# Kernel tuning notes

Hardware: AMD Instinct MI355X
Metric: run time of the kernel (lower is better)

## Reference

```python
import jax, jax.numpy as jnp
import numpy as np

H = 16  # num_heads (matches init_kwargs)


def setup_inputs() -> dict:
    key = jax.random.key(0)
    ks = jax.random.split(key, 5)
    B, T, C = 4, 2048, 2048
    S = C // H
    g = 0.5 * (6.0 / (C + C)) ** 0.5 * (3.0 ** 0.5)  # ~xavier_uniform scale, gain 0.5
    x = jax.random.normal(ks[0], (B, T, C), dtype=jnp.float32)
    Wk = jax.random.uniform(ks[1], (C, C), jnp.float32, -g, g)
    Wv = jax.random.uniform(ks[2], (C, C), jnp.float32, -g, g)
    Wr = jax.random.uniform(ks[3], (C, C), jnp.float32, -g, g)
    Wo = jax.random.uniform(ks[4], (C, C), jnp.float32, -g, g)
    time_decay = jnp.full((H, S), -5.0, dtype=jnp.float32)
    time_first = jnp.zeros((H, S), dtype=jnp.float32)
    return {"x": x, "Wk": Wk, "Wv": Wv, "Wr": Wr, "Wo": Wo,
            "time_decay": time_decay, "time_first": time_first}


def _wkv(k, v, time_decay, time_first):
    # k, v: [B, T, H, S] float32
    decay = jnp.exp(-jnp.exp(time_decay.astype(jnp.float32)))  # [H, S]
    first = jnp.exp(time_first.astype(jnp.float32))            # [H, S]
    w = jnp.exp(jnp.clip(k.astype(jnp.float32), -10.0, 10.0))  # [B, T, H, S]
    # t==0 branch (state = first*w0*v0) == uniform recurrence with w0 scaled by first
    w = w.at[:, 0].multiply(first)
    wt = jnp.swapaxes(w, 0, 1)                    # [T, B, H, S]
    vt = jnp.swapaxes(v.astype(jnp.float32), 0, 1)

    def step(carry, inp):
        num, den = carry
        w_t, v_t = inp
        num = decay * num + w_t * v_t
        den = decay * den + w_t
        return (num, den), num / (den + 1e-6)

    B, _, _, S = k.shape
    init = (jnp.zeros((B, H, S), jnp.float32), jnp.zeros((B, H, S), jnp.float32))
    _, wkv = jax.lax.scan(step, init, (wt, vt))   # [T, B, H, S]
    return jnp.swapaxes(wkv, 0, 1).astype(k.dtype)  # [B, T, H, S]


def reference(x, Wk, Wv, Wr, Wo, time_decay, time_first):
    B, T, C = x.shape
    S = C // H
    k = (x @ Wk.T).reshape(B, T, H, S)
    v = (x @ Wv.T).reshape(B, T, H, S)
    r = (x @ Wr.T).reshape(B, T, H, S)
    wkv = _wkv(k, v, time_decay, time_first)
    rwkv = (jax.nn.sigmoid(r) * wkv).reshape(B, T, C)
    return rwkv @ Wo.T
```

## Files before the change

### kernel.cpp

```cpp
#include <hip/hip_runtime.h>
#include <hip/hip_bf16.h>

using bf16 = __hip_bfloat16;
using floatx4 = __attribute__((ext_vector_type(4))) float;
using bf16x8  = __attribute__((ext_vector_type(8))) __bf16;
using bf16x2  = __attribute__((ext_vector_type(2))) __bf16;

#define MDIM 8192
#define NDIM 2048
#define KDIM 2048
#define TSEQ 2048
#define BB   4
#define CDIM 2048
#define NCHUNK 64
#define TCHUNK 32

typedef __attribute__((address_space(1))) void gvoid_t;
typedef __attribute__((address_space(3))) void lvoid_t;

__device__ __forceinline__ void load_lds16(const void* g, void* l) {
  __builtin_amdgcn_global_load_lds((gvoid_t*)(void*)g, (lvoid_t*)l, 16, 0, 0);
}

__global__ __launch_bounds__(256) void cvt_all(
    const float* __restrict__ x,
    const float* __restrict__ Wk, const float* __restrict__ Wv,
    const float* __restrict__ Wr, const float* __restrict__ Wo,
    __bf16* __restrict__ xb,
    __bf16* __restrict__ wkb, __bf16* __restrict__ wvb,
    __bf16* __restrict__ wrb, __bf16* __restrict__ wob) {
  const size_t WN = (size_t)NDIM * KDIM;
  const int slice = blockIdx.y;
  const float* s;
  __bf16* d;
  if (slice < 4) { s = x + (size_t)slice * WN; d = xb + (size_t)slice * WN; }
  else {
    s = (slice == 4) ? Wk : (slice == 5) ? Wv : (slice == 6) ? Wr : Wo;
    d = (slice == 4) ? wkb : (slice == 5) ? wvb : (slice == 6) ? wrb : wob;
  }
  const int i = (blockIdx.x * 256 + threadIdx.x) * 8;
  float4 a = *(const float4*)(s + i);
  float4 b = *(const float4*)(s + i + 4);
  bf16x8 o;
  o[0] = (__bf16)a.x; o[1] = (__bf16)a.y; o[2] = (__bf16)a.z; o[3] = (__bf16)a.w;
  o[4] = (__bf16)b.x; o[5] = (__bf16)b.y; o[6] = (__bf16)b.z; o[7] = (__bf16)b.w;
  *(bf16x8*)(d + i) = o;
}


#define GBARRIER() asm volatile("s_barrier" ::: "memory")
#define VMW8()     asm volatile("s_waitcnt vmcnt(8)" ::: "memory")
#define VMW4()     asm volatile("s_waitcnt vmcnt(4)" ::: "memory")
#define VMW0()     asm volatile("s_waitcnt vmcnt(0)" ::: "memory")

template <typename CT>
__device__ __forceinline__ void gemm256_body(const __bf16* __restrict__ A,
                                             const __bf16* __restrict__ B,
                                             CT* __restrict__ C,
                                             const int bm, const int bn) {
  __shared__ __attribute__((aligned(128))) unsigned char lds[131072];
  const int tid  = threadIdx.x;
  const int lane = tid & 63;
  const int wave = tid >> 6;
  const int wm = wave >> 2;
  const int wn = wave & 3;

  floatx4 acc[8][4] = {};
  bf16x8 af[8], bfr[2];

  const int srow = tid >> 2;
  const int scol = ((tid & 3) ^ ((tid >> 3) & 3)) * 8;
  const __bf16* Ag = A + (size_t)(bm * 256 + srow) * KDIM + scol;
  const __bf16* Bg = B + (size_t)(bn * 256 + srow) * KDIM + scol;
  const uint32_t sdst = (uint32_t)tid * 16u;

  const uint32_t laneoff =
      (uint32_t)((lane & 15) * 64 + (((lane >> 4) ^ ((lane >> 1) & 3)) * 16));
  const uint32_t aoff = (uint32_t)(wm * 8192) + laneoff;
  const uint32_t boff = 16384u + (uint32_t)(wn * 4096) + laneoff;

#define BUF(t_) ((uint32_t)((t_) & 3) * 32768u)
#define STG_A(t_) {                                                           \
  load_lds16(Ag + (size_t)(t_) * 32,                                          \
             (void*)(lds + BUF(t_) + sdst));                                  \
  load_lds16(Ag + (size_t)128 * KDIM + (size_t)(t_) * 32,                     \
             (void*)(lds + BUF(t_) + 8192u + sdst)); }
#define STG_B(t_) {                                                           \
  load_lds16(Bg + (size_t)(t_) * 32,                                          \
             (void*)(lds + BUF(t_) + 16384u + sdst));                         \
  load_lds16(Bg + (size_t)128 * KDIM + (size_t)(t_) * 32,                     \
             (void*)(lds + BUF(t_) + 24576u + sdst)); }
#define RD_AF(bo_) {                                                          \
  const uint32_t ab = (bo_) + aoff;                                           \
  af[0] = *(const bf16x8*)(lds + ab);        af[1] = *(const bf16x8*)(lds + ab + 1024); \
  af[2] = *(const bf16x8*)(lds + ab + 2048); af[3] = *(const bf16x8*)(lds + ab + 3072); \
  af[4] = *(const bf16x8*)(lds + ab + 4096); af[5] = *(const bf16x8*)(lds + ab + 5120); \
  af[6] = *(const bf16x8*)(lds + ab + 6144); af[7] = *(const bf16x8*)(lds + ab + 7168); }
#define RD_BF(bo_, nh_) {                                                     \
  const uint32_t bb = (bo_) + boff + (nh_) * 2048u;                           \
  bfr[0] = *(const bf16x8*)(lds + bb);                                        \
  bfr[1] = *(const bf16x8*)(lds + bb + 1024); }
#define MFMA16(j0_) {                                                         \
  __builtin_amdgcn_s_setprio(1);                                              \
  _Pragma("unroll")                                                           \
  for (int m_ = 0; m_ < 8; ++m_) {                                            \
    acc[m_][(j0_)]     = __builtin_amdgcn_mfma_f32_16x16x32_bf16(af[m_], bfr[0], acc[m_][(j0_)], 0, 0, 0);     \
    acc[m_][(j0_) + 1] = __builtin_amdgcn_mfma_f32_16x16x32_bf16(af[m_], bfr[1], acc[m_][(j0_) + 1], 0, 0, 0); \
  }                                                                           \
  __builtin_amdgcn_s_setprio(0); }

  STG_A(0); STG_B(0);
  STG_A(1); STG_B(1);
  STG_A(2); STG_B(2);
  VMW8();
  GBARRIER();

  constexpr int NT = KDIM / 32;
  for (int t = 0; t < NT - 3; ++t) {
    const uint32_t bo = BUF(t);
    RD_AF(bo); RD_BF(bo, 0);
    STG_A(t + 3);
    MFMA16(0);
    RD_BF(bo, 1);
    STG_B(t + 3);
    MFMA16(2);
    VMW8();
    GBARRIER();
  }
  {
    const uint32_t bo = BUF(NT - 3);
    RD_AF(bo); RD_BF(bo, 0);
    MFMA16(0);
    RD_BF(bo, 1);
    MFMA16(2);
    VMW4();
    GBARRIER();
  }
  {
    const uint32_t bo = BUF(NT - 2);
    RD_AF(bo); RD_BF(bo, 0);
    MFMA16(0);
    RD_BF(bo, 1);
    MFMA16(2);
    VMW0();
    GBARRIER();
  }
  {
    const uint32_t bo = BUF(NT - 1);
    RD_AF(bo); RD_BF(bo, 0);
    MFMA16(0);
    RD_BF(bo, 1);
    MFMA16(2);
  }

  const int crow = (lane >> 4) * 4;
  const int ccol = lane & 15;
#pragma unroll
  for (int i = 0; i < 8; ++i)
#pragma unroll
    for (int j = 0; j < 4; ++j) {
      const size_t r0 = (size_t)(bm * 256 + wm * 128 + i * 16 + crow);
      const int    c0 = bn * 256 + wn * 64 + j * 16 + ccol;
#pragma unroll
      for (int rg = 0; rg < 4; ++rg)
        C[(r0 + rg) * NDIM + c0] = (CT)(acc[i][j][rg]);
    }
#undef BUF
#undef STG_A
#undef STG_B
#undef RD_AF
#undef RD_BF
#undef MFMA16
}

__device__ __forceinline__ void xcd_swz(int& bm, int& bn) {
  const int f = (int)(blockIdx.y * 32 + blockIdx.x);
  const int s = (f & 7) * 32 + (f >> 3);
  bm = s & 31;
  bn = s >> 5;
}

__global__ __launch_bounds__(512, 2) void gemm_qkv(const __bf16* __restrict__ x,
                                                   const __bf16* __restrict__ Wk,
                                                   const __bf16* __restrict__ Wv,
                                                   const __bf16* __restrict__ Wr,
                                                   __bf16* __restrict__ kb,
                                                   __bf16* __restrict__ vb,
                                                   __bf16* __restrict__ rb) {
  const __bf16* Bsel = (blockIdx.z == 0) ? Wk : (blockIdx.z == 1) ? Wv : Wr;
  __bf16*       Csel = (blockIdx.z == 0) ? kb : (blockIdx.z == 1) ? vb : rb;
  int bm, bn; xcd_swz(bm, bn);
  gemm256_body<__bf16>(x, Bsel, Csel, bm, bn);
}

__global__ __launch_bounds__(512, 2) void gemm_o(const __bf16* __restrict__ A,
                                                 const __bf16* __restrict__ B,
                                                 float* __restrict__ C) {
  int bm, bn; xcd_swz(bm, bn);
  gemm256_body<float>(A, B, C, bm, bn);
}

__global__ __launch_bounds__(256) void wkv_summary(
    const __bf16* __restrict__ kb, const __bf16* __restrict__ vb,
    const float* __restrict__ td, const float* __restrict__ tf,
    float* __restrict__ nsum, float* __restrict__ dsum) {
  const int c0 = (blockIdx.x * 256 + threadIdx.x) * 2;
  const int chunk = blockIdx.y;
  const int b = blockIdx.z;
  const float dc0 = __expf(-__expf(td[c0]));
  const float dc1 = __expf(-__expf(td[c0 + 1]));
  const float fi0 = __expf(tf[c0]);
  const float fi1 = __expf(tf[c0 + 1]);
  size_t base = ((size_t)b * TSEQ + (size_t)chunk * TCHUNK) * CDIM + c0;
  float n0 = 0.f, d0 = 0.f, n1 = 0.f, d1 = 0.f;
#pragma unroll 4
  for (int t = 0; t < TCHUNK; ++t) {
    bf16x2 k2 = *(const bf16x2*)(kb + base + (size_t)t * CDIM);
    bf16x2 v2 = *(const bf16x2*)(vb + base + (size_t)t * CDIM);
    float k0f = fminf(fmaxf((float)k2[0], -10.f), 10.f);
    float k1f = fminf(fmaxf((float)k2[1], -10.f), 10.f);
    float w0 = __expf(k0f), w1 = __expf(k1f);
    if (chunk == 0 && t == 0) { w0 *= fi0; w1 *= fi1; }
    n0 = dc0 * n0 + w0 * (float)v2[0];
    d0 = dc0 * d0 + w0;
    n1 = dc1 * n1 + w1 * (float)v2[1];
    d1 = dc1 * d1 + w1;
  }
  const size_t si = (size_t)(chunk * BB + b) * CDIM + c0;
  *(float2*)(nsum + si) = make_float2(n0, n1);
  *(float2*)(dsum + si) = make_float2(d0, d1);
}

__global__ __launch_bounds__(256) void wkv_scan(
    const float* __restrict__ td,
    float* __restrict__ nsum, float* __restrict__ dsum) {
  const int c0 = (blockIdx.x * 256 + threadIdx.x) * 2;
  const int b = blockIdx.y;
  const float dT0 = __expf(-__expf(td[c0]) * (float)TCHUNK);
  const float dT1 = __expf(-__expf(td[c0 + 1]) * (float)TCHUNK);
  float pn0 = 0.f, pd0 = 0.f, pn1 = 0.f, pd1 = 0.f;
  for (int j = 0; j < NCHUNK; ++j) {
    const size_t si = (size_t)(j * BB + b) * CDIM + c0;
    float2 Sn = *(const float2*)(nsum + si);
    float2 Sd = *(const float2*)(dsum + si);
    *(float2*)(nsum + si) = make_float2(pn0, pn1);
    *(float2*)(dsum + si) = make_float2(pd0, pd1);
    pn0 = dT0 * pn0 + Sn.x;  pn1 = dT1 * pn1 + Sn.y;
    pd0 = dT0 * pd0 + Sd.x;  pd1 = dT1 * pd1 + Sd.y;
  }
}

__global__ __launch_bounds__(256) void wkv_apply(
    const __bf16* __restrict__ kb, const __bf16* __restrict__ vb,
    __bf16* __restrict__ rb,
    const float* __restrict__ td, const float* __restrict__ tf,
    const float* __restrict__ nsum, const float* __restrict__ dsum) {
  const int c0 = (blockIdx.x * 256 + threadIdx.x) * 2;
  const int chunk = blockIdx.y;
  const int b = blockIdx.z;
  const float dc0 = __expf(-__expf(td[c0]));
  const float dc1 = __expf(-__expf(td[c0 + 1]));
  const float fi0 = __expf(tf[c0]);
  const float fi1 = __expf(tf[c0 + 1]);

  const size_t si = (size_t)(chunk * BB + b) * CDIM + c0;
  float2 pn = *(const float2*)(nsum + si);
  float2 pd = *(const float2*)(dsum + si);
  float n0 = pn.x, n1 = pn.y, d0 = pd.x, d1 = pd.y;

  size_t base = ((size_t)b * TSEQ + (size_t)chunk * TCHUNK) * CDIM + c0;
#pragma unroll 2
  for (int t = 0; t < TCHUNK; ++t) {
    const size_t idx = base + (size_t)t * CDIM;
    bf16x2 k2 = *(const bf16x2*)(kb + idx);
    bf16x2 v2 = *(const bf16x2*)(vb + idx);
    bf16x2 r2 = *(const bf16x2*)(rb + idx);
    float k0f = fminf(fmaxf((float)k2[0], -10.f), 10.f);
    float k1f = fminf(fmaxf((float)k2[1], -10.f), 10.f);
    float w0 = __expf(k0f), w1 = __expf(k1f);
    if (chunk == 0 && t == 0) { w0 *= fi0; w1 *= fi1; }
    n0 = dc0 * n0 + w0 * (float)v2[0];
    d0 = dc0 * d0 + w0;
    n1 = dc1 * n1 + w1 * (float)v2[1];
    d1 = dc1 * d1 + w1;
    const float wkv0 = n0 * __builtin_amdgcn_rcpf(d0 + 1e-6f);
    const float wkv1 = n1 * __builtin_amdgcn_rcpf(d1 + 1e-6f);
    const float sr0 = __builtin_amdgcn_rcpf(1.f + __expf(-(float)r2[0]));
    const float sr1 = __builtin_amdgcn_rcpf(1.f + __expf(-(float)r2[1]));
    bf16x2 o;
    o[0] = (__bf16)(sr0 * wkv0);
    o[1] = (__bf16)(sr1 * wkv1);
    *(bf16x2*)(rb + idx) = o;
  }
}

extern "C" void kernel_launch(void* const* d_in, const int* in_sizes, int n_in,
                              void* d_out, int out_size, void* d_ws, size_t ws_size,
                              hipStream_t stream) {
  const float* x  = (const float*)d_in[0];
  const float* Wk = (const float*)d_in[1];
  const float* Wv = (const float*)d_in[2];
  const float* Wr = (const float*)d_in[3];
  const float* Wo = (const float*)d_in[4];
  const float* td = (const float*)d_in[5];
  const float* tf = (const float*)d_in[6];
  float* out = (float*)d_out;

  char* ws = (char*)d_ws;
  const size_t matX = (size_t)MDIM * KDIM * sizeof(__bf16);
  const size_t matW = (size_t)NDIM * KDIM * sizeof(__bf16);
  __bf16* xb  = (__bf16*)(ws);
  __bf16* wkb = (__bf16*)(ws + matX);
  __bf16* wvb = (__bf16*)(ws + matX + matW);
  __bf16* wrb = (__bf16*)(ws + matX + 2 * matW);
  __bf16* wob = (__bf16*)(ws + matX + 3 * matW);
  __bf16* kb  = (__bf16*)(ws + matX + 4 * matW);
  __bf16* vb  = (__bf16*)(ws + 2 * matX + 4 * matW);
  __bf16* rb  = (__bf16*)(ws + 3 * matX + 4 * matW);
  float* nsum = (float*)(ws + 4 * matX + 4 * matW);
  float* dsum = nsum + (size_t)NCHUNK * BB * CDIM;

  dim3 blk(256);
  dim3 blk5(512);
  cvt_all<<<dim3(NDIM * KDIM / (8 * 256), 8), blk, 0, stream>>>(
      x, Wk, Wv, Wr, Wo, xb, wkb, wvb, wrb, wob);

  dim3 gq(MDIM / 256, NDIM / 256, 3);
  gemm_qkv<<<gq, blk5, 0, stream>>>(xb, wkb, wvb, wrb, kb, vb, rb);
  dim3 gw(CDIM / 512, NCHUNK, BB);
  wkv_summary<<<gw, blk, 0, stream>>>(kb, vb, td, tf, nsum, dsum);
  wkv_scan<<<dim3(CDIM / 512, BB), blk, 0, stream>>>(td, nsum, dsum);
  wkv_apply<<<gw, blk, 0, stream>>>(kb, vb, rb, td, tf, nsum, dsum);
  dim3 go(MDIM / 256, NDIM / 256, 1);
  gemm_o<<<go, blk5, 0, stream>>>(rb, wob, out);
}
```

Measured before the change: 465.8 us.

## Use 4-wave 256x256 GEMM tiles with 128x128 per-wave output

Rebuilds the shared 256x256 bf16 GEMM body so that 4 waves (256 threads) cover the tile instead of 8. Each wave now computes a 128x128 sub-tile with 8x8 MFMA accumulators and reads 8 B fragments per k-step, which raises MFMA work per LDS read. Each thread issues 4 global-to-LDS loads per operand, and the vmcnt waits are adjusted to match. The cost is twice the accumulator registers (256 VGPRs of accumulators) and one block per CU, which risks register spilling and leaves less latency hiding.

```diff
diff --git a/kernel.cpp b/kernel.cpp
--- a/kernel.cpp
+++ b/kernel.cpp
@@ -49,8 +49,8 @@
 
 
 #define GBARRIER() asm volatile("s_barrier" ::: "memory")
+#define VMW16()    asm volatile("s_waitcnt vmcnt(16)" ::: "memory")
 #define VMW8()     asm volatile("s_waitcnt vmcnt(8)" ::: "memory")
-#define VMW4()     asm volatile("s_waitcnt vmcnt(4)" ::: "memory")
 #define VMW0()     asm volatile("s_waitcnt vmcnt(0)" ::: "memory")
 
 template <typename CT>
@@ -62,11 +62,11 @@
   const int tid  = threadIdx.x;
   const int lane = tid & 63;
   const int wave = tid >> 6;
-  const int wm = wave >> 2;
-  const int wn = wave & 3;
-
-  floatx4 acc[8][4] = {};
-  bf16x8 af[8], bfr[2];
+  const int wm = wave >> 1;
+  const int wn = wave & 1;
+
+  floatx4 acc[8][8] = {};
+  bf16x8 af[8], bfr[8];
 
   const int srow = tid >> 2;
   const int scol = ((tid & 3) ^ ((tid >> 3) & 3)) * 8;
@@ -77,80 +77,78 @@
   const uint32_t laneoff =
       (uint32_t)((lane & 15) * 64 + (((lane >> 4) ^ ((lane >> 1) & 3)) * 16));
   const uint32_t aoff = (uint32_t)(wm * 8192) + laneoff;
-  const uint32_t boff = 16384u + (uint32_t)(wn * 4096) + laneoff;
+  const uint32_t boff = 16384u + (uint32_t)(wn * 8192) + laneoff;
 
 #define BUF(t_) ((uint32_t)((t_) & 3) * 32768u)
 #define STG_A(t_) {                                                           \
-  load_lds16(Ag + (size_t)(t_) * 32,                                          \
-             (void*)(lds + BUF(t_) + sdst));                                  \
-  load_lds16(Ag + (size_t)128 * KDIM + (size_t)(t_) * 32,                     \
-             (void*)(lds + BUF(t_) + 8192u + sdst)); }
+  _Pragma("unroll")                                                           \
+  for (int q_ = 0; q_ < 4; ++q_)                                              \
+    load_lds16(Ag + (size_t)(q_ * 64) * KDIM + (size_t)(t_) * 32,             \
+               (void*)(lds + BUF(t_) + (uint32_t)q_ * 4096u + sdst)); }
 #define STG_B(t_) {                                                           \
-  load_lds16(Bg + (size_t)(t_) * 32,                                          \
-             (void*)(lds + BUF(t_) + 16384u + sdst));                         \
-  load_lds16(Bg + (size_t)128 * KDIM + (size_t)(t_) * 32,                     \
-             (void*)(lds + BUF(t_) + 24576u + sdst)); }
+  _Pragma("unroll")                                                           \
+  for (int q_ = 0; q_ < 4; ++q_)                                              \
+    load_lds16(Bg + (size_t)(q_ * 64) * KDIM + (size_t)(t_) * 32,             \
+               (void*)(lds + BUF(t_) + 16384u + (uint32_t)q_ * 4096u + sdst)); }
 #define RD_AF(bo_) {                                                          \
   const uint32_t ab = (bo_) + aoff;                                           \
-  af[0] = *(const bf16x8*)(lds + ab);        af[1] = *(const bf16x8*)(lds + ab + 1024); \
-  af[2] = *(const bf16x8*)(lds + ab + 2048); af[3] = *(const bf16x8*)(lds + ab + 3072); \
-  af[4] = *(const bf16x8*)(lds + ab + 4096); af[5] = *(const bf16x8*)(lds + ab + 5120); \
-  af[6] = *(const bf16x8*)(lds + ab + 6144); af[7] = *(const bf16x8*)(lds + ab + 7168); }
-#define RD_BF(bo_, nh_) {                                                     \
-  const uint32_t bb = (bo_) + boff + (nh_) * 2048u;                           \
-  bfr[0] = *(const bf16x8*)(lds + bb);                                        \
-  bfr[1] = *(const bf16x8*)(lds + bb + 1024); }
-#define MFMA16(j0_) {                                                         \
+  _Pragma("unroll")                                                           \
+  for (int i_ = 0; i_ < 8; ++i_)                                              \
+    af[i_] = *(const bf16x8*)(lds + ab + (uint32_t)i_ * 1024u); }
+#define RD_BF(bo_) {                                                          \
+  const uint32_t bb = (bo_) + boff;                                           \
+  _Pragma("unroll")                                                           \
+  for (int j_ = 0; j_ < 8; ++j_)                                              \
+    bfr[j_] = *(const bf16x8*)(lds + bb + (uint32_t)j_ * 1024u); }
+#define MFMA32(J0_) {                                                         \
   __builtin_amdgcn_s_setprio(1);                                              \
   _Pragma("unroll")                                                           \
-  for (int m_ = 0; m_ < 8; ++m_) {                                            \
-    acc[m_][(j0_)]     = __builtin_amdgcn_mfma_f32_16x16x32_bf16(af[m_], bfr[0], acc[m_][(j0_)], 0, 0, 0);     \
-    acc[m_][(j0_) + 1] = __builtin_amdgcn_mfma_f32_16x16x32_bf16(af[m_], bfr[1], acc[m_][(j0_) + 1], 0, 0, 0); \
+  for (int j_ = (J0_); j_ < (J0_) + 4; ++j_) {                                \
+    _Pragma("unroll")                                                         \
+    for (int m_ = 0; m_ < 8; ++m_)                                            \
+      acc[m_][j_] = __builtin_amdgcn_mfma_f32_16x16x32_bf16(                  \
+          af[m_], bfr[j_], acc[m_][j_], 0, 0, 0);                             \
   }                                                                           \
   __builtin_amdgcn_s_setprio(0); }
 
   STG_A(0); STG_B(0);
   STG_A(1); STG_B(1);
   STG_A(2); STG_B(2);
-  VMW8();
+  VMW16();
   GBARRIER();
 
   constexpr int NT = KDIM / 32;
   for (int t = 0; t < NT - 3; ++t) {
     const uint32_t bo = BUF(t);
-    RD_AF(bo); RD_BF(bo, 0);
+    RD_AF(bo); RD_BF(bo);
     STG_A(t + 3);
-    MFMA16(0);
-    RD_BF(bo, 1);
+    MFMA32(0);
     STG_B(t + 3);
-    MFMA16(2);
+    MFMA32(4);
+    VMW16();
+    GBARRIER();
+  }
+  {
+    const uint32_t bo = BUF(NT - 3);
+    RD_AF(bo); RD_BF(bo);
+    MFMA32(0);
+    MFMA32(4);
     VMW8();
     GBARRIER();
   }
   {
-    const uint32_t bo = BUF(NT - 3);
-    RD_AF(bo); RD_BF(bo, 0);
-    MFMA16(0);
-    RD_BF(bo, 1);
-    MFMA16(2);
-    VMW4();
-    GBARRIER();
-  }
-  {
     const uint32_t bo = BUF(NT - 2);
-    RD_AF(bo); RD_BF(bo, 0);
-    MFMA16(0);
-    RD_BF(bo, 1);
-    MFMA16(2);
+    RD_AF(bo); RD_BF(bo);
+    MFMA32(0);
+    MFMA32(4);
     VMW0();
     GBARRIER();
   }
   {
     const uint32_t bo = BUF(NT - 1);
-    RD_AF(bo); RD_BF(bo, 0);
-    MFMA16(0);
-    RD_BF(bo, 1);
-    MFMA16(2);
+    RD_AF(bo); RD_BF(bo);
+    MFMA32(0);
+    MFMA32(4);
   }
 
   const int crow = (lane >> 4) * 4;
@@ -158,9 +156,9 @@
 #pragma unroll
   for (int i = 0; i < 8; ++i)
 #pragma unroll
-    for (int j = 0; j < 4; ++j) {
+    for (int j = 0; j < 8; ++j) {
       const size_t r0 = (size_t)(bm * 256 + wm * 128 + i * 16 + crow);
-      const int    c0 = bn * 256 + wn * 64 + j * 16 + ccol;
+      const int    c0 = bn * 256 + wn * 128 + j * 16 + ccol;
 #pragma unroll
       for (int rg = 0; rg < 4; ++rg)
         C[(r0 + rg) * NDIM + c0] = (CT)(acc[i][j][rg]);
@@ -170,7 +168,7 @@
 #undef STG_B
 #undef RD_AF
 #undef RD_BF
-#undef MFMA16
+#undef MFMA32
 }
 
 __device__ __forceinline__ void xcd_swz(int& bm, int& bn) {
@@ -180,7 +178,7 @@
   bn = s >> 5;
 }
 
-__global__ __launch_bounds__(512, 2) void gemm_qkv(const __bf16* __restrict__ x,
+__global__ __launch_bounds__(256, 1) void gemm_qkv(const __bf16* __restrict__ x,
                                                    const __bf16* __restrict__ Wk,
                                                    const __bf16* __restrict__ Wv,
                                                    const __bf16* __restrict__ Wr,
@@ -193,7 +191,7 @@
   gemm256_body<__bf16>(x, Bsel, Csel, bm, bn);
 }
 
-__global__ __launch_bounds__(512, 2) void gemm_o(const __bf16* __restrict__ A,
+__global__ __launch_bounds__(256, 1) void gemm_o(const __bf16* __restrict__ A,
                                                  const __bf16* __restrict__ B,
                                                  float* __restrict__ C) {
   int bm, bn; xcd_swz(bm, bn);
@@ -321,16 +319,15 @@
   float* dsum = nsum + (size_t)NCHUNK * BB * CDIM;
 
   dim3 blk(256);
-  dim3 blk5(512);
   cvt_all<<<dim3(NDIM * KDIM / (8 * 256), 8), blk, 0, stream>>>(
       x, Wk, Wv, Wr, Wo, xb, wkb, wvb, wrb, wob);
 
   dim3 gq(MDIM / 256, NDIM / 256, 3);
-  gemm_qkv<<<gq, blk5, 0, stream>>>(xb, wkb, wvb, wrb, kb, vb, rb);
+  gemm_qkv<<<gq, blk, 0, stream>>>(xb, wkb, wvb, wrb, kb, vb, rb);
   dim3 gw(CDIM / 512, NCHUNK, BB);
   wkv_summary<<<gw, blk, 0, stream>>>(kb, vb, td, tf, nsum, dsum);
   wkv_scan<<<dim3(CDIM / 512, BB), blk, 0, stream>>>(td, nsum, dsum);
   wkv_apply<<<gw, blk, 0, stream>>>(kb, vb, rb, td, tf, nsum, dsum);
   dim3 go(MDIM / 256, NDIM / 256, 1);
-  gemm_o<<<go, blk5, 0, stream>>>(rb, wob, out);
-}
+  gemm_o<<<go, blk, 0, stream>>>(rb, wob, out);
+}
```

New measurement: 497.3 us. +6.8%, slower.
